# Performance work log

Hardware: AMD Instinct MI355X
Metric: run time of the kernel (lower is better)

The kernel has to match this reference:

```python
import jax, jax.numpy as jnp
import numpy as np

N_NODES = 50000
N_EDGES = 800000
N_GRAPHS = 128
IN_DIM = 256
OUT_DIM = 128
N_LAYERS = 3
NEG_SLOPE = 0.01  # nn.LeakyReLU default


def setup_inputs() -> dict:
    key = jax.random.key(0)
    ks = jax.random.split(key, 10)
    feat = jax.random.normal(ks[0], (N_NODES, IN_DIM), jnp.float32)
    src = jax.random.randint(ks[1], (N_EDGES,), 0, N_NODES, jnp.int32)
    dst = jax.random.randint(ks[2], (N_EDGES,), 0, N_NODES, jnp.int32)
    graph_ids = jnp.sort(jax.random.randint(ks[3], (N_NODES,), 0, N_GRAPHS, jnp.int32))
    s_in = 1.0 / np.sqrt(IN_DIM).astype(np.float32)
    s_out = 1.0 / np.sqrt(OUT_DIM).astype(np.float32)
    w_red = jax.random.uniform(ks[4], (IN_DIM, OUT_DIM), jnp.float32, -s_in, s_in)
    b_red = jax.random.uniform(ks[5], (OUT_DIM,), jnp.float32, -s_in, s_in)
    w_gcn = jax.random.uniform(ks[6], (N_LAYERS, OUT_DIM, OUT_DIM), jnp.float32, -s_out, s_out)
    b_gcn = jnp.zeros((N_LAYERS, OUT_DIM), jnp.float32)  # DGL GraphConv bias init = zeros
    w_cls = jax.random.uniform(ks[7], (OUT_DIM, 2), jnp.float32, -s_out, s_out)
    b_cls = jax.random.uniform(ks[8], (2,), jnp.float32, -s_out, s_out)
    return dict(feat=feat, src=src, dst=dst, graph_ids=graph_ids,
                w_red=w_red, b_red=b_red, w_gcn=w_gcn, b_gcn=b_gcn,
                w_cls=w_cls, b_cls=b_cls)


def _graph_conv(x, src, dst, w, b, out_norm, in_norm):
    # DGL GraphConv, norm='both': h = D_in^{-1/2} A D_out^{-1/2} x W + b
    xs = x * out_norm[:, None]                                   # [N, d] source normalization
    agg = jax.ops.segment_sum(xs[src], dst, num_segments=x.shape[0])  # gather -> scatter-add
    return (agg * in_norm[:, None]) @ w + b


def reference(feat, src, dst, graph_ids, w_red, b_red, w_gcn, b_gcn, w_cls, b_cls):
    n = feat.shape[0]
    ones = jnp.ones((src.shape[0],), feat.dtype)
    out_deg = jax.ops.segment_sum(ones, src, num_segments=n)
    in_deg = jax.ops.segment_sum(ones, dst, num_segments=n)
    out_norm = jnp.maximum(out_deg, 1.0) ** -0.5  # DGL clamps degree to >=1
    in_norm = jnp.maximum(in_deg, 1.0) ** -0.5
    h0 = feat @ w_red + b_red  # Dropout(0.2) in eval mode = identity
    # Faithful to source: every layer consumes h0 (node_features never updated);
    # only the last layer's activation survives the loop.
    out = h0
    for i in range(N_LAYERS):
        out = jax.nn.leaky_relu(
            _graph_conv(h0, src, dst, w_gcn[i], b_gcn[i], out_norm, in_norm), NEG_SLOPE)
    g = jax.ops.segment_sum(out, graph_ids, num_segments=N_GRAPHS)  # sum readout per graph
    return g @ w_cls + b_cls  # [N_GRAPHS, 2]
```

## Files before the change

kernel.cpp:

```cpp
#include <hip/hip_runtime.h>

#define N_NODES 50000
#define N_EDGES 800000
#define N_GRAPHS 128
#define IN_DIM 256
#define OUT_DIM 128
#define NEG_SLOPE 0.01f

#define RCHUNK 64
#define NB_SCAN ((N_NODES + 255) / 256)

#define NSLICE 4
#define SLICE 12544
#define NTOT (NSLICE * SLICE)
#define NCHUNK 64
#define NE4 (N_EDGES / 4)
#define QPC (NE4 / NCHUNK)

typedef __attribute__((ext_vector_type(8))) short bf16x8;
typedef __attribute__((ext_vector_type(4))) float f32x4;
typedef unsigned short ushort_t;
typedef unsigned int uint_t;

__device__ inline ushort_t f2b(float f) {
    union { float f; unsigned u; } c{f};
    unsigned r = c.u + 0x7FFFu + ((c.u >> 16) & 1u);
    return (ushort_t)(r >> 16);
}
__device__ inline float b2f(ushort_t u) {
    union { unsigned u; float f; } c{(unsigned)u << 16};
    return c.f;
}
__device__ inline float blo(uint_t v) {
    union { unsigned u; float f; } c{v << 16};
    return c.f;
}
__device__ inline float bhi(uint_t v) {
    union { unsigned u; float f; } c{v & 0xFFFF0000u};
    return c.f;
}

__global__ __launch_bounds__(256) void deg_kernel(const int4* __restrict__ src4,
                                                  const int4* __restrict__ dst4,
                                                  ushort_t* __restrict__ rep) {
    __shared__ int bins[SLICE];
    int b     = blockIdx.x;
    int hist  = b >> 8;
    int rem   = b & 255;
    int slice = rem >> 6;
    int chunk = rem & 63;
    const int4* ea = hist ? dst4 : src4;
    int lo = slice * SLICE;

    for (int i = threadIdx.x; i < SLICE; i += 256) bins[i] = 0;
    __syncthreads();

    int q0 = chunk * QPC;
    int q1 = q0 + QPC;
    for (int q = q0 + threadIdx.x; q < q1; q += 256) {
        int4 e = ea[q];
        unsigned a0 = (unsigned)(e.x - lo); if (a0 < SLICE) atomicAdd(&bins[a0], 1);
        unsigned a1 = (unsigned)(e.y - lo); if (a1 < SLICE) atomicAdd(&bins[a1], 1);
        unsigned a2 = (unsigned)(e.z - lo); if (a2 < SLICE) atomicAdd(&bins[a2], 1);
        unsigned a3 = (unsigned)(e.w - lo); if (a3 < SLICE) atomicAdd(&bins[a3], 1);
    }
    __syncthreads();

    uint_t* rp32 = (uint_t*)(rep + (size_t)(hist * NCHUNK + chunk) * NTOT + lo);
    for (int i = threadIdx.x; i < SLICE / 2; i += 256)
        rp32[i] = (uint_t)(bins[2 * i] | (bins[2 * i + 1] << 16));
}

__global__ __launch_bounds__(256) void norm_kernel(ushort_t* __restrict__ rep,
                                                   float* __restrict__ out_norm,
                                                   float* __restrict__ in_norm,
                                                   int* __restrict__ deg_in_tot,
                                                   int* __restrict__ bsum) {
    __shared__ int red[256];
    int t = threadIdx.x;
    int i = blockIdx.x * 256 + t;
    int si_keep = 0;
    if (i < N_NODES) {
        int so = 0;
#pragma unroll
        for (int c = 0; c < NCHUNK; ++c) so += rep[(size_t)c * NTOT + i];
        int si = 0;
#pragma unroll
        for (int c = 0; c < NCHUNK; ++c) {
            size_t off = (size_t)(NCHUNK + c) * NTOT + i;
            int v = rep[off];
            rep[off] = (ushort_t)si;
            si += v;
        }
        deg_in_tot[i] = si;
        si_keep = si;
        int dq = so > 1 ? so : 1;
        int di = si > 1 ? si : 1;
        out_norm[i] = rsqrtf((float)dq);
        in_norm[i]  = rsqrtf((float)di);
    }
    red[t] = si_keep;
    __syncthreads();
    for (int off = 128; off > 0; off >>= 1) {
        if (t < off) red[t] += red[t + off];
        __syncthreads();
    }
    if (t == 0) bsum[blockIdx.x] = red[0];
}

__global__ __launch_bounds__(256) void scan_bsums(const int* __restrict__ bsum,
                                                  int* __restrict__ bofs,
                                                  int* __restrict__ row_ofs) {
    __shared__ int sh[256];
    int t = threadIdx.x;
    int v = (t < NB_SCAN) ? bsum[t] : 0;
    sh[t] = v;
    __syncthreads();
    for (int off = 1; off < 256; off <<= 1) {
        int a = sh[t];
        int b = (t >= off) ? sh[t - off] : 0;
        __syncthreads();
        sh[t] = a + b;
        __syncthreads();
    }
    if (t < NB_SCAN) bofs[t] = sh[t] - v;
    if (t == 255)    row_ofs[N_NODES] = sh[NB_SCAN - 1];
}

__global__ __launch_bounds__(256) void fill_kernel(const int* __restrict__ deg_in,
                                                   const int* __restrict__ bofs,
                                                   int* __restrict__ row_ofs) {
    __shared__ int sh[256];
    int t   = threadIdx.x;
    int idx = blockIdx.x * 256 + t;
    int v   = (idx < N_NODES) ? deg_in[idx] : 0;
    sh[t] = v;
    __syncthreads();
    for (int off = 1; off < 256; off <<= 1) {
        int a = sh[t];
        int b = (t >= off) ? sh[t - off] : 0;
        __syncthreads();
        sh[t] = a + b;
        __syncthreads();
    }
    if (idx < N_NODES) row_ofs[idx] = bofs[blockIdx.x] + sh[t] - v;
}

__global__ __launch_bounds__(256) void build_kernel(const int4* __restrict__ src4,
                                                    const int4* __restrict__ dst4,
                                                    const int* __restrict__ row_ofs,
                                                    const ushort_t* __restrict__ rep,
                                                    int* __restrict__ esrc) {
    __shared__ int cur[SLICE];
    int b     = blockIdx.x;
    int slice = b >> 6;
    int chunk = b & 63;
    int lo    = slice * SLICE;
    const ushort_t* rel = rep + (size_t)(NCHUNK + chunk) * NTOT + lo;

    for (int i = threadIdx.x; i < SLICE; i += 256) {
        int n = lo + i;
        int r = (n < N_NODES) ? row_ofs[n] : 0;
        cur[i] = r + (int)rel[i];
    }
    __syncthreads();

    int q0 = chunk * QPC;
    int q1 = q0 + QPC;
    for (int q = q0 + threadIdx.x; q < q1; q += 256) {
        int4 s = src4[q];
        int4 d = dst4[q];
        unsigned a0 = (unsigned)(d.x - lo); if (a0 < SLICE) esrc[atomicAdd(&cur[a0], 1)] = s.x;
        unsigned a1 = (unsigned)(d.y - lo); if (a1 < SLICE) esrc[atomicAdd(&cur[a1], 1)] = s.y;
        unsigned a2 = (unsigned)(d.z - lo); if (a2 < SLICE) esrc[atomicAdd(&cur[a2], 1)] = s.z;
        unsigned a3 = (unsigned)(d.w - lo); if (a3 < SLICE) esrc[atomicAdd(&cur[a3], 1)] = s.w;
    }
}

__global__ __launch_bounds__(128) void wc_kernel(const float* __restrict__ w_red,
                                                 const float* __restrict__ b_red,
                                                 const float* __restrict__ w2,
                                                 ushort_t* __restrict__ Wcs,
                                                 float* __restrict__ bc) {
    int j = threadIdx.x;
    int i = blockIdx.x;
    const float* vin = (i < IN_DIM) ? (w_red + (size_t)i * OUT_DIM) : b_red;
    float s = 0.f;
    for (int k = 0; k < OUT_DIM; ++k) s = fmaf(vin[k], w2[k * OUT_DIM + j], s);
    if (i < IN_DIM) Wcs[(size_t)j * IN_DIM + i] = f2b(s);
    else            bc[j] = s;
}

__global__ __launch_bounds__(256) void gemm_z(const float* __restrict__ feat,
                                              const ushort_t* __restrict__ Wcs,
                                              const float* __restrict__ bc,
                                              const float* __restrict__ out_norm,
                                              ushort_t* __restrict__ zb) {
    __shared__ ushort_t Bs[64 * IN_DIM];
    int t    = threadIdx.x;
    int lane = t & 63;
    int wv   = t >> 6;
    int bm   = blockIdx.x * 64 + wv * 16;
    int bn0  = blockIdx.y * 64;
    int mrow = lane & 15;
    int kg   = lane >> 4;
    int gm   = bm + mrow;

    {
        const char* wsrc = (const char*)(Wcs + (size_t)bn0 * IN_DIM);
        char* bdst = (char*)Bs;
#pragma unroll
        for (int p = 0; p < 8; ++p) {
            int d  = p * 4096 + t * 16;
            int ds = d ^ (((d >> 9) & 7) << 4);
            *(int4*)(bdst + ds) = *(const int4*)(wsrc + d);
        }
    }
    __syncthreads();

    f32x4 acc[4];
#pragma unroll
    for (int nt = 0; nt < 4; ++nt) acc[nt] = (f32x4){0.f, 0.f, 0.f, 0.f};

    int boff[4];
#pragma unroll
    for (int nt = 0; nt < 4; ++nt) {
        int n = nt * 16 + mrow;
        boff[nt] = n * 512 + ((kg * 16) ^ ((n & 7) << 4));
    }
    const char* bsp = (const char*)Bs;

    bool valid = gm < N_NODES;
    const float* fp = feat + (size_t)(valid ? gm : 0) * IN_DIM + kg * 8;
    const float4 zf4 = make_float4(0.f, 0.f, 0.f, 0.f);

    float4 a0c = valid ? *(const float4*)(fp + 0) : zf4;
    float4 a1c = valid ? *(const float4*)(fp + 4) : zf4;
    float4 a0n = zf4, a1n = zf4;

#pragma unroll
    for (int kt = 0; kt < IN_DIM / 32; ++kt) {
        if (kt < IN_DIM / 32 - 1) {
            a0n = valid ? *(const float4*)(fp + (kt + 1) * 32) : zf4;
            a1n = valid ? *(const float4*)(fp + (kt + 1) * 32 + 4) : zf4;
        }
        bf16x8 af;
        af[0] = (short)f2b(a0c.x); af[1] = (short)f2b(a0c.y);
        af[2] = (short)f2b(a0c.z); af[3] = (short)f2b(a0c.w);
        af[4] = (short)f2b(a1c.x); af[5] = (short)f2b(a1c.y);
        af[6] = (short)f2b(a1c.z); af[7] = (short)f2b(a1c.w);
#pragma unroll
        for (int nt = 0; nt < 4; ++nt) {
            bf16x8 bf = *(const bf16x8*)(bsp + (boff[nt] ^ (kt << 6)));
            acc[nt] = __builtin_amdgcn_mfma_f32_16x16x32_bf16(af, bf, acc[nt], 0, 0, 0);
        }
        a0c = a0n; a1c = a1n;
    }

    float on[4];
#pragma unroll
    for (int r = 0; r < 4; ++r) {
        int row = bm + kg * 4 + r;
        on[r] = (row < N_NODES) ? out_norm[row] : 0.f;
    }
#pragma unroll
    for (int nt = 0; nt < 4; ++nt) {
        int col = bn0 + nt * 16 + mrow;
        float bcv = bc[col];
#pragma unroll
        for (int r = 0; r < 4; ++r) {
            int row = bm + kg * 4 + r;
            if (row < N_NODES)
                zb[(size_t)row * OUT_DIM + col] = f2b(on[r] * (acc[nt][r] + bcv));
        }
    }
}

__global__ __launch_bounds__(256) void gather_kernel(const uint4* __restrict__ zb4,
                                                     const int* __restrict__ esrc,
                                                     const int* __restrict__ row_ofs,
                                                     const float* __restrict__ in_norm,
                                                     const float* __restrict__ b2,
                                                     uint4* __restrict__ hb4) {
    int n      = blockIdx.x * 16 + (threadIdx.x >> 4);
    int lane16 = threadIdx.x & 15;
    int e0 = row_ofs[n];
    int e1 = row_ofs[n + 1];
    float ac[8];
#pragma unroll
    for (int i = 0; i < 8; ++i) ac[i] = 0.f;

    int e = e0;
    for (; e + 4 <= e1; e += 4) {
        int sa = esrc[e + 0];
        int sb = esrc[e + 1];
        int sc = esrc[e + 2];
        int sd = esrc[e + 3];
        uint4 va = zb4[(size_t)sa * 16 + lane16];
        uint4 vb = zb4[(size_t)sb * 16 + lane16];
        uint4 vc = zb4[(size_t)sc * 16 + lane16];
        uint4 vd = zb4[(size_t)sd * 16 + lane16];
        ac[0] += (blo(va.x) + blo(vb.x)) + (blo(vc.x) + blo(vd.x));
        ac[1] += (bhi(va.x) + bhi(vb.x)) + (bhi(vc.x) + bhi(vd.x));
        ac[2] += (blo(va.y) + blo(vb.y)) + (blo(vc.y) + blo(vd.y));
        ac[3] += (bhi(va.y) + bhi(vb.y)) + (bhi(vc.y) + bhi(vd.y));
        ac[4] += (blo(va.z) + blo(vb.z)) + (blo(vc.z) + blo(vd.z));
        ac[5] += (bhi(va.z) + bhi(vb.z)) + (bhi(vc.z) + bhi(vd.z));
        ac[6] += (blo(va.w) + blo(vb.w)) + (blo(vc.w) + blo(vd.w));
        ac[7] += (bhi(va.w) + bhi(vb.w)) + (bhi(vc.w) + bhi(vd.w));
    }
    for (; e < e1; ++e) {
        uint4 v = zb4[(size_t)esrc[e] * 16 + lane16];
        ac[0] += blo(v.x); ac[1] += bhi(v.x);
        ac[2] += blo(v.y); ac[3] += bhi(v.y);
        ac[4] += blo(v.z); ac[5] += bhi(v.z);
        ac[6] += blo(v.w); ac[7] += bhi(v.w);
    }

    float inn = in_norm[n];
    float4 bA = *(const float4*)&b2[lane16 * 8];
    float4 bB = *(const float4*)&b2[lane16 * 8 + 4];
    float hv[8];
    hv[0] = fmaf(inn, ac[0], bA.x); hv[1] = fmaf(inn, ac[1], bA.y);
    hv[2] = fmaf(inn, ac[2], bA.z); hv[3] = fmaf(inn, ac[3], bA.w);
    hv[4] = fmaf(inn, ac[4], bB.x); hv[5] = fmaf(inn, ac[5], bB.y);
    hv[6] = fmaf(inn, ac[6], bB.z); hv[7] = fmaf(inn, ac[7], bB.w);
#pragma unroll
    for (int i = 0; i < 8; ++i) hv[i] = (hv[i] > 0.f) ? hv[i] : NEG_SLOPE * hv[i];
    uint4 o;
    o.x = (uint_t)f2b(hv[0]) | ((uint_t)f2b(hv[1]) << 16);
    o.y = (uint_t)f2b(hv[2]) | ((uint_t)f2b(hv[3]) << 16);
    o.z = (uint_t)f2b(hv[4]) | ((uint_t)f2b(hv[5]) << 16);
    o.w = (uint_t)f2b(hv[6]) | ((uint_t)f2b(hv[7]) << 16);
    hb4[(size_t)n * 16 + lane16] = o;
}

__global__ __launch_bounds__(128) void readout_kernel(const ushort_t* __restrict__ hb,
                                                      const int* __restrict__ gids,
                                                      float* __restrict__ g) {
    int j    = threadIdx.x;
    int n0   = blockIdx.x * RCHUNK;
    int nend = n0 + RCHUNK;
    if (nend > N_NODES) nend = N_NODES;
    float acc = 0.f;
    int   cur = gids[n0];
    for (int n = n0; n < nend; ++n) {
        int gid = gids[n];
        if (gid != cur) {
            atomicAdd(&g[cur * OUT_DIM + j], acc);
            acc = 0.f;
            cur = gid;
        }
        acc += b2f(hb[(size_t)n * OUT_DIM + j]);
    }
    atomicAdd(&g[cur * OUT_DIM + j], acc);
}

__global__ __launch_bounds__(256) void cls_kernel(const float* __restrict__ g,
                                                  const float* __restrict__ w_cls,
                                                  const float* __restrict__ b_cls,
                                                  float* __restrict__ out) {
    int t  = threadIdx.x;
    int gr = t >> 1;
    int c  = t & 1;
    float s = b_cls[c];
    for (int k = 0; k < OUT_DIM; ++k) s = fmaf(g[gr * OUT_DIM + k], w_cls[k * 2 + c], s);
    out[t] = s;
}

extern "C" void kernel_launch(void* const* d_in, const int* in_sizes, int n_in,
                              void* d_out, int out_size, void* d_ws, size_t ws_size,
                              hipStream_t stream) {
    const float* feat  = (const float*)d_in[0];
    const int*   src   = (const int*)d_in[1];
    const int*   dst   = (const int*)d_in[2];
    const int*   gids  = (const int*)d_in[3];
    const float* w_red = (const float*)d_in[4];
    const float* b_red = (const float*)d_in[5];
    const float* w_gcn = (const float*)d_in[6];
    const float* b_gcn = (const float*)d_in[7];
    const float* w_cls = (const float*)d_in[8];
    const float* b_cls = (const float*)d_in[9];
    float* out = (float*)d_out;

    float* z        = (float*)d_ws;
    float* h        = z + (size_t)N_NODES * OUT_DIM;
    float* out_norm = h + (size_t)N_NODES * OUT_DIM;
    float* in_norm  = out_norm + N_NODES;
    int*   deg_in   = (int*)(in_norm + N_NODES);
    int*   row_ofs  = deg_in + N_NODES;
    int*   esrc     = row_ofs + N_NODES + 1;
    int*   bsum     = esrc + N_EDGES;
    int*   bofs     = bsum + NB_SCAN;
    ushort_t* Wcs   = (ushort_t*)(bofs + NB_SCAN);
    float* bc       = (float*)(Wcs + IN_DIM * OUT_DIM);
    float* g        = bc + OUT_DIM;

    ushort_t* zb = (ushort_t*)z;
    ushort_t* hb = (ushort_t*)h;

    ushort_t* rep = (ushort_t*)z;

    const float* w2 = w_gcn + 2 * OUT_DIM * OUT_DIM;
    const float* b2 = b_gcn + 2 * OUT_DIM;

    hipMemsetAsync(g, 0, (size_t)N_GRAPHS * OUT_DIM * sizeof(float), stream);

    deg_kernel<<<2 * NSLICE * NCHUNK, 256, 0, stream>>>((const int4*)src, (const int4*)dst, rep);
    norm_kernel<<<NB_SCAN, 256, 0, stream>>>(rep, out_norm, in_norm, deg_in, bsum);
    scan_bsums<<<1, 256, 0, stream>>>(bsum, bofs, row_ofs);
    fill_kernel<<<NB_SCAN, 256, 0, stream>>>(deg_in, bofs, row_ofs);
    build_kernel<<<NSLICE * NCHUNK, 256, 0, stream>>>((const int4*)src, (const int4*)dst,
                                                      row_ofs, rep, esrc);
    wc_kernel<<<IN_DIM + 1, OUT_DIM, 0, stream>>>(w_red, b_red, w2, Wcs, bc);
    gemm_z<<<dim3((N_NODES + 63) / 64, 2), 256, 0, stream>>>(feat, Wcs, bc, out_norm, zb);
    gather_kernel<<<N_NODES / 16, 256, 0, stream>>>((const uint4*)zb, esrc, row_ofs,
                                                    in_norm, b2, (uint4*)hb);
    readout_kernel<<<(N_NODES + RCHUNK - 1) / RCHUNK, 128, 0, stream>>>(hb, gids, g);
    cls_kernel<<<1, 256, 0, stream>>>(g, w_cls, b_cls, out);
}
```

Baseline: 162.7 us.

## Fuse block-sum scan into fill, deepen gather unroll, vectorize readout loads

The single-block scan_bsums kernel is folded into fill_kernel: every block redundantly scans the 196 block sums to get its own offset, which removes one launch and its serial dependency. The gather loop issues 8 independent row loads per iteration instead of 4, exposing more memory-level parallelism at the cost of more registers. The readout kernel uses 64 threads that each load a packed pair of bf16 values and issue two atomics, halving the thread count per block.

```diff
diff --git a/kernel.cpp b/kernel.cpp
--- a/kernel.cpp
+++ b/kernel.cpp
@@ -108,11 +108,13 @@
     if (t == 0) bsum[blockIdx.x] = red[0];
 }
 
-__global__ __launch_bounds__(256) void scan_bsums(const int* __restrict__ bsum,
-                                                  int* __restrict__ bofs,
-                                                  int* __restrict__ row_ofs) {
+__global__ __launch_bounds__(256) void fill_kernel(const int* __restrict__ deg_in,
+                                                   const int* __restrict__ bsum,
+                                                   int* __restrict__ row_ofs) {
     __shared__ int sh[256];
-    int t = threadIdx.x;
+    int t   = threadIdx.x;
+    int bid = blockIdx.x;
+
     int v = (t < NB_SCAN) ? bsum[t] : 0;
     sh[t] = v;
     __syncthreads();
@@ -123,18 +125,13 @@
         sh[t] = a + b;
         __syncthreads();
     }
-    if (t < NB_SCAN) bofs[t] = sh[t] - v;
-    if (t == 255)    row_ofs[N_NODES] = sh[NB_SCAN - 1];
-}
-
-__global__ __launch_bounds__(256) void fill_kernel(const int* __restrict__ deg_in,
-                                                   const int* __restrict__ bofs,
-                                                   int* __restrict__ row_ofs) {
-    __shared__ int sh[256];
-    int t   = threadIdx.x;
-    int idx = blockIdx.x * 256 + t;
-    int v   = (idx < N_NODES) ? deg_in[idx] : 0;
-    sh[t] = v;
+    int bofs  = sh[bid] - bsum[bid];
+    int total = sh[NB_SCAN - 1];
+    __syncthreads();
+
+    int idx = bid * 256 + t;
+    int dv  = (idx < N_NODES) ? deg_in[idx] : 0;
+    sh[t] = dv;
     __syncthreads();
     for (int off = 1; off < 256; off <<= 1) {
         int a = sh[t];
@@ -143,7 +140,8 @@
         sh[t] = a + b;
         __syncthreads();
     }
-    if (idx < N_NODES) row_ofs[idx] = bofs[blockIdx.x] + sh[t] - v;
+    if (idx < N_NODES) row_ofs[idx] = bofs + sh[t] - dv;
+    if (bid == 0 && t == 0) row_ofs[N_NODES] = total;
 }
 
 __global__ __launch_bounds__(256) void build_kernel(const int4* __restrict__ src4,
@@ -291,23 +289,30 @@
     for (int i = 0; i < 8; ++i) ac[i] = 0.f;
 
     int e = e0;
-    for (; e + 4 <= e1; e += 4) {
-        int sa = esrc[e + 0];
-        int sb = esrc[e + 1];
-        int sc = esrc[e + 2];
-        int sd = esrc[e + 3];
-        uint4 va = zb4[(size_t)sa * 16 + lane16];
-        uint4 vb = zb4[(size_t)sb * 16 + lane16];
-        uint4 vc = zb4[(size_t)sc * 16 + lane16];
-        uint4 vd = zb4[(size_t)sd * 16 + lane16];
-        ac[0] += (blo(va.x) + blo(vb.x)) + (blo(vc.x) + blo(vd.x));
-        ac[1] += (bhi(va.x) + bhi(vb.x)) + (bhi(vc.x) + bhi(vd.x));
-        ac[2] += (blo(va.y) + blo(vb.y)) + (blo(vc.y) + blo(vd.y));
-        ac[3] += (bhi(va.y) + bhi(vb.y)) + (bhi(vc.y) + bhi(vd.y));
-        ac[4] += (blo(va.z) + blo(vb.z)) + (blo(vc.z) + blo(vd.z));
-        ac[5] += (bhi(va.z) + bhi(vb.z)) + (bhi(vc.z) + bhi(vd.z));
-        ac[6] += (blo(va.w) + blo(vb.w)) + (blo(vc.w) + blo(vd.w));
-        ac[7] += (bhi(va.w) + bhi(vb.w)) + (bhi(vc.w) + bhi(vd.w));
+    for (; e + 8 <= e1; e += 8) {
+        uint4 v[8];
+#pragma unroll
+        for (int u = 0; u < 8; ++u) v[u] = zb4[(size_t)esrc[e + u] * 16 + lane16];
+#pragma unroll
+        for (int u = 0; u < 8; ++u) {
+            ac[0] += blo(v[u].x); ac[1] += bhi(v[u].x);
+            ac[2] += blo(v[u].y); ac[3] += bhi(v[u].y);
+            ac[4] += blo(v[u].z); ac[5] += bhi(v[u].z);
+            ac[6] += blo(v[u].w); ac[7] += bhi(v[u].w);
+        }
+    }
+    if (e + 4 <= e1) {
+        uint4 v[4];
+#pragma unroll
+        for (int u = 0; u < 4; ++u) v[u] = zb4[(size_t)esrc[e + u] * 16 + lane16];
+#pragma unroll
+        for (int u = 0; u < 4; ++u) {
+            ac[0] += blo(v[u].x); ac[1] += bhi(v[u].x);
+            ac[2] += blo(v[u].y); ac[3] += bhi(v[u].y);
+            ac[4] += blo(v[u].z); ac[5] += bhi(v[u].z);
+            ac[6] += blo(v[u].w); ac[7] += bhi(v[u].w);
+        }
+        e += 4;
     }
     for (; e < e1; ++e) {
         uint4 v = zb4[(size_t)esrc[e] * 16 + lane16];
@@ -335,25 +340,29 @@
     hb4[(size_t)n * 16 + lane16] = o;
 }
 
-__global__ __launch_bounds__(128) void readout_kernel(const ushort_t* __restrict__ hb,
-                                                      const int* __restrict__ gids,
-                                                      float* __restrict__ g) {
-    int j    = threadIdx.x;
+__global__ __launch_bounds__(64) void readout_kernel(const uint_t* __restrict__ hb2,
+                                                     const int* __restrict__ gids,
+                                                     float* __restrict__ g) {
+    int t    = threadIdx.x;
     int n0   = blockIdx.x * RCHUNK;
     int nend = n0 + RCHUNK;
     if (nend > N_NODES) nend = N_NODES;
-    float acc = 0.f;
+    float acc0 = 0.f, acc1 = 0.f;
     int   cur = gids[n0];
     for (int n = n0; n < nend; ++n) {
         int gid = gids[n];
         if (gid != cur) {
-            atomicAdd(&g[cur * OUT_DIM + j], acc);
-            acc = 0.f;
+            atomicAdd(&g[cur * OUT_DIM + 2 * t], acc0);
+            atomicAdd(&g[cur * OUT_DIM + 2 * t + 1], acc1);
+            acc0 = acc1 = 0.f;
             cur = gid;
         }
-        acc += b2f(hb[(size_t)n * OUT_DIM + j]);
-    }
-    atomicAdd(&g[cur * OUT_DIM + j], acc);
+        uint_t v = hb2[(size_t)n * 64 + t];
+        acc0 += blo(v);
+        acc1 += bhi(v);
+    }
+    atomicAdd(&g[cur * OUT_DIM + 2 * t], acc0);
+    atomicAdd(&g[cur * OUT_DIM + 2 * t + 1], acc1);
 }
 
 __global__ __launch_bounds__(256) void cls_kernel(const float* __restrict__ g,
@@ -391,8 +400,7 @@
     int*   row_ofs  = deg_in + N_NODES;
     int*   esrc     = row_ofs + N_NODES + 1;
     int*   bsum     = esrc + N_EDGES;
-    int*   bofs     = bsum + NB_SCAN;
-    ushort_t* Wcs   = (ushort_t*)(bofs + NB_SCAN);
+    ushort_t* Wcs   = (ushort_t*)(bsum + NB_SCAN);
     float* bc       = (float*)(Wcs + IN_DIM * OUT_DIM);
     float* g        = bc + OUT_DIM;
 
@@ -408,14 +416,14 @@
 
     deg_kernel<<<2 * NSLICE * NCHUNK, 256, 0, stream>>>((const int4*)src, (const int4*)dst, rep);
     norm_kernel<<<NB_SCAN, 256, 0, stream>>>(rep, out_norm, in_norm, deg_in, bsum);
-    scan_bsums<<<1, 256, 0, stream>>>(bsum, bofs, row_ofs);
-    fill_kernel<<<NB_SCAN, 256, 0, stream>>>(deg_in, bofs, row_ofs);
+    fill_kernel<<<NB_SCAN, 256, 0, stream>>>(deg_in, bsum, row_ofs);
     build_kernel<<<NSLICE * NCHUNK, 256, 0, stream>>>((const int4*)src, (const int4*)dst,
                                                       row_ofs, rep, esrc);
     wc_kernel<<<IN_DIM + 1, OUT_DIM, 0, stream>>>(w_red, b_red, w2, Wcs, bc);
     gemm_z<<<dim3((N_NODES + 63) / 64, 2), 256, 0, stream>>>(feat, Wcs, bc, out_norm, zb);
     gather_kernel<<<N_NODES / 16, 256, 0, stream>>>((const uint4*)zb, esrc, row_ofs,
                                                     in_norm, b2, (uint4*)hb);
-    readout_kernel<<<(N_NODES + RCHUNK - 1) / RCHUNK, 128, 0, stream>>>(hb, gids, g);
+    readout_kernel<<<(N_NODES + RCHUNK - 1) / RCHUNK, 64, 0, stream>>>((const uint_t*)hb,
+                                                                       gids, g);
     cls_kernel<<<1, 256, 0, stream>>>(g, w_cls, b_cls, out);
 }
```

Result: no change. 163.6 us (+0.6%).
